# Kernel optimization log

Measured on AMD Instinct MI355X. Metric: run time of the kernel, lower is better.

## Reference

```python
import jax, jax.numpy as jnp
import numpy as np

EMB = 128
N_LIG = 32768
N_REC = 262144
NUM_GRAPHS = 1024
E_LIG = 327680
E_REC = 2097152
LIG_DIMS = [119, 9, 11, 12, 9, 5, 8, 2, 2]
NUM_LAYERS = 3
BN_EPS = 1e-5


def setup_inputs() -> dict:
    key = jax.random.key(0)
    ks = iter(jax.random.split(key, 64))

    lig_x = jnp.stack(
        [jax.random.randint(next(ks), (N_LIG,), 0, d) for d in LIG_DIMS], axis=1
    )  # [N_lig, 9] categorical atom features
    atom_offsets = jnp.asarray(np.cumsum([0] + LIG_DIMS[:-1]), dtype=jnp.int32)
    atom_emb = jax.random.normal(next(ks), (sum(LIG_DIMS), EMB), jnp.float32) * 0.1

    rec_x_int = jax.random.randint(next(ks), (N_REC,), 0, 20)
    rec_x_float = jax.random.normal(next(ks), (N_REC, 199), jnp.float32)
    rec_emb1 = jax.random.normal(next(ks), (20, EMB), jnp.float32) * 0.1
    rec_w = jax.random.normal(next(ks), (199, EMB), jnp.float32) * 0.05
    rec_b = jnp.zeros((EMB,), jnp.float32)

    lig_edge_index = jax.random.randint(next(ks), (2, E_LIG), 0, N_LIG)
    rec_edge_index = jax.random.randint(next(ks), (2, E_REC), 0, N_REC)
    lig_batch = jnp.repeat(jnp.arange(NUM_GRAPHS), N_LIG // NUM_GRAPHS)
    rec_batch = jnp.repeat(jnp.arange(NUM_GRAPHS), N_REC // NUM_GRAPHS)

    def layer_params():
        W = jax.random.normal(next(ks), (NUM_LAYERS, EMB, EMB), jnp.float32) * (1.0 / np.sqrt(EMB))
        b = jnp.zeros((NUM_LAYERS, EMB), jnp.float32)
        gamma = jnp.ones((NUM_LAYERS, EMB), jnp.float32)
        beta = jnp.zeros((NUM_LAYERS, EMB), jnp.float32)
        return W, b, gamma, beta

    lig_W, lig_b, lig_gamma, lig_beta = layer_params()
    rec_W, rec_bc, rec_gamma, rec_beta = layer_params()

    out_w1 = jax.random.normal(next(ks), (2 * EMB, EMB), jnp.float32) * (1.0 / np.sqrt(2 * EMB))
    out_b1 = jnp.zeros((EMB,), jnp.float32)
    out_w2 = jax.random.normal(next(ks), (EMB, 1), jnp.float32) * (1.0 / np.sqrt(EMB))
    out_b2 = jnp.zeros((1,), jnp.float32)

    return dict(
        lig_x=lig_x, rec_x_int=rec_x_int, rec_x_float=rec_x_float,
        lig_edge_index=lig_edge_index, rec_edge_index=rec_edge_index,
        lig_batch=lig_batch, rec_batch=rec_batch, atom_offsets=atom_offsets,
        atom_emb=atom_emb, rec_emb1=rec_emb1, rec_w=rec_w, rec_b=rec_b,
        lig_W=lig_W, lig_b=lig_b, lig_gamma=lig_gamma, lig_beta=lig_beta,
        rec_W=rec_W, rec_bc=rec_bc, rec_gamma=rec_gamma, rec_beta=rec_beta,
        out_w1=out_w1, out_b1=out_b1, out_w2=out_w2, out_b2=out_b2,
    )


def gcn_layer(x, edge_index, W, b, gamma, beta):
    """GCNConv (sym-norm, self loops) -> BatchNorm (batch stats) -> ReLU."""
    n = x.shape[0]
    h = x @ W  # [N, EMB]
    loops = jnp.arange(n)
    src = jnp.concatenate([edge_index[0], loops])
    dst = jnp.concatenate([edge_index[1], loops])
    deg = jax.ops.segment_sum(jnp.ones_like(dst, dtype=h.dtype), dst, num_segments=n)
    dinv = jax.lax.rsqrt(jnp.maximum(deg, 1.0))  # deg >= 1 with self loops
    msg = h[src] * (dinv[src] * dinv[dst])[:, None]  # gather + normalize
    out = jax.ops.segment_sum(msg, dst, num_segments=n) + b
    mu = out.mean(axis=0)
    var = out.var(axis=0)
    out = (out - mu) * jax.lax.rsqrt(var + BN_EPS) * gamma + beta
    return jax.nn.relu(out)


def scatter_mean(x, seg, num_segments):
    s = jax.ops.segment_sum(x, seg, num_segments=num_segments)
    cnt = jax.ops.segment_sum(jnp.ones((x.shape[0],), x.dtype), seg, num_segments=num_segments)
    return s / jnp.maximum(cnt, 1.0)[:, None]


def reference(lig_x, rec_x_int, rec_x_float, lig_edge_index, rec_edge_index,
              lig_batch, rec_batch, atom_offsets, atom_emb, rec_emb1, rec_w, rec_b,
              lig_W, lig_b, lig_gamma, lig_beta, rec_W, rec_bc, rec_gamma, rec_beta,
              out_w1, out_b1, out_w2, out_b2):
    # Node encoders
    lig_h = atom_emb[lig_x + atom_offsets[None, :]].sum(axis=1)        # [N_lig, EMB]
    rec_h = rec_emb1[rec_x_int] + rec_x_float @ rec_w + rec_b          # [N_rec, EMB]

    for l in range(NUM_LAYERS):
        lig_h = gcn_layer(lig_h, lig_edge_index, lig_W[l], lig_b[l], lig_gamma[l], lig_beta[l])
        rec_h = gcn_layer(rec_h, rec_edge_index, rec_W[l], rec_bc[l], rec_gamma[l], rec_beta[l])

    lig_feat = scatter_mean(lig_h, lig_batch, NUM_GRAPHS)
    rec_feat = scatter_mean(rec_h, rec_batch, NUM_GRAPHS)
    z = jnp.concatenate([lig_feat, rec_feat], axis=1)                  # [B, 2*EMB]
    z = jax.nn.relu(z @ out_w1 + out_b1)
    return (z @ out_w2 + out_b2).squeeze(-1)                            # [B]
```

## Files before the change

kernel.cpp:

```cpp
#include <hip/hip_runtime.h>
#include <hip/hip_bf16.h>
#include <cstdint>
#include <cstddef>

#define EMB 128
#define NLIG 32768
#define NREC 262144
#define NGRAPH 1024
#define ELIG 327680
#define EREC 2097152
#define BN_EPS 1e-5f

typedef unsigned short ushort_t;
typedef short bf16x8 __attribute__((ext_vector_type(8)));
typedef float f32x4 __attribute__((ext_vector_type(4)));

__device__ __forceinline__ float bf2f(ushort_t u) {
  union { unsigned int i; float f; } v;
  v.i = ((unsigned int)u) << 16;
  return v.f;
}
__device__ __forceinline__ ushort_t f2bf(float f) {
  __hip_bfloat16 h = __float2bfloat16(f);
  union { __hip_bfloat16 h; ushort_t u; } v;
  v.h = h;
  return v.u;
}


__global__ __launch_bounds__(256)
void gk_count(const int* __restrict__ dst, int* __restrict__ cnt, int E) {
  int e = blockIdx.x * 256 + threadIdx.x;
  if (e < E) atomicAdd(&cnt[dst[e]], 1);
}

__global__ __launch_bounds__(256)
void gk_scan1(const int* __restrict__ cnt, int* __restrict__ off,
              int* __restrict__ bsum, int n) {
  __shared__ int sm[256];
  int t = threadIdx.x;
  int base = blockIdx.x * 1024 + t * 4;
  int v0 = (base + 0 < n) ? cnt[base + 0] : 0;
  int v1 = (base + 1 < n) ? cnt[base + 1] : 0;
  int v2 = (base + 2 < n) ? cnt[base + 2] : 0;
  int v3 = (base + 3 < n) ? cnt[base + 3] : 0;
  int loc = v0 + v1 + v2 + v3;
  sm[t] = loc;
  __syncthreads();
  for (int o = 1; o < 256; o <<= 1) {
    int x = (t >= o) ? sm[t - o] : 0;
    __syncthreads();
    sm[t] += x;
    __syncthreads();
  }
  int run = sm[t] - loc;
  if (base + 0 < n) off[base + 0] = run;
  run += v0;
  if (base + 1 < n) off[base + 1] = run;
  run += v1;
  if (base + 2 < n) off[base + 2] = run;
  run += v2;
  if (base + 3 < n) off[base + 3] = run;
  if (t == 255) bsum[blockIdx.x] = sm[255];
}

__global__ __launch_bounds__(256)
void gk_scan2(int* __restrict__ bsum, int nb) {
  __shared__ int sm[256];
  int t = threadIdx.x;
  int v = (t < nb) ? bsum[t] : 0;
  sm[t] = v;
  __syncthreads();
  for (int o = 1; o < 256; o <<= 1) {
    int x = (t >= o) ? sm[t - o] : 0;
    __syncthreads();
    sm[t] += x;
    __syncthreads();
  }
  if (t < nb) bsum[t] = sm[t] - v;
}

__global__ __launch_bounds__(256)
void gk_scan3f(int* __restrict__ off, const int* __restrict__ bsum,
               int* __restrict__ cur, float* __restrict__ dinv, int n, int E) {
  int i = blockIdx.x * 256 + threadIdx.x;
  if (i < n) {
    int deg = cur[i];
    int o = off[i] + bsum[i >> 10];
    off[i] = o;
    cur[i] = o;
    dinv[i] = rsqrtf((float)(deg + 1));
  }
  if (i == 0) off[n] = E;
}

__global__ __launch_bounds__(256)
void gk_fill(const int* __restrict__ src, const int* __restrict__ dst,
             int* __restrict__ cur, int* __restrict__ csr, int E) {
  int e = blockIdx.x * 256 + threadIdx.x;
  if (e < E) {
    int d = dst[e];
    int pos = atomicAdd(&cur[d], 1);
    csr[pos] = src[e];
  }
}


__global__ __launch_bounds__(256)
void gk_recw2(const float* __restrict__ W, ushort_t* __restrict__ Wt) {
  int idx = blockIdx.x * 256 + threadIdx.x;
  if (idx < 128 * 224) {
    int c = idx / 224, k = idx - c * 224;
    Wt[idx] = (k < 199) ? f2bf(W[(size_t)k * 128 + c]) : (ushort_t)0;
  }
}

__global__ __launch_bounds__(256)
void gk_xcast(const float* __restrict__ X, ushort_t* __restrict__ Xb) {
  const int ITEMS = NREC * 25;
  int stride = gridDim.x * 256;
  for (int v = blockIdx.x * 256 + threadIdx.x; v < ITEMS; v += stride) {
    int row = v / 25, sub = v - row * 25;
    int k0 = sub * 8;
    const float* xr = X + (size_t)row * 199 + k0;
    ushort_t tmp[8];
#pragma unroll
    for (int j = 0; j < 8; ++j) {
      float f = (k0 + j < 199) ? xr[j] : 0.f;
      tmp[j] = f2bf(f);
    }
    *(uint4*)(Xb + (size_t)row * 200 + k0) = *(uint4*)tmp;
  }
}

#define LIGB (NLIG / 2)
__global__ __launch_bounds__(256)
void gk_enc2(const int* __restrict__ lig_x, const int* __restrict__ offs,
             const float* __restrict__ emb,
             const ushort_t* __restrict__ Xb, const int* __restrict__ xi,
             const float* __restrict__ emb1, const ushort_t* __restrict__ Wt,
             const float* __restrict__ b,
             ushort_t* __restrict__ Al, ushort_t* __restrict__ Ar) {
  int t = threadIdx.x;
  if (blockIdx.x < LIGB) {
    __shared__ int idx[2][9];
    int n0 = blockIdx.x * 2;
    if (t < 9) idx[0][t] = lig_x[n0 * 9 + t] + offs[t];
    else if (t >= 128 && t < 137) idx[1][t - 128] = lig_x[(n0 + 1) * 9 + (t - 128)] + offs[t - 128];
    __syncthreads();
    int half = t >> 7, c = t & 127;
    float acc = 0.f;
#pragma unroll
    for (int f = 0; f < 9; ++f) acc += emb[(size_t)idx[half][f] * EMB + c];
    Al[(size_t)(n0 + half) * EMB + c] = f2bf(acc);
    return;
  }
  int row0 = (blockIdx.x - LIGB) * 128;
  int w = t >> 6, lane = t & 63;
  int m = lane & 15, quad = lane >> 4;
  int rbase = w * 32;
  int rA = row0 + rbase + m;
  int rB = rA + 16;

  f32x4 acc[2][8];
#pragma unroll
  for (int rt = 0; rt < 2; ++rt)
#pragma unroll
    for (int ct = 0; ct < 8; ++ct) acc[rt][ct] = (f32x4){0.f, 0.f, 0.f, 0.f};

  const ushort_t* xpA = Xb + (size_t)rA * 200 + quad * 8;
  const ushort_t* xpB = Xb + (size_t)rB * 200 + quad * 8;
  const ushort_t* wp = Wt + (size_t)m * 224 + quad * 8;

  for (int ch = 0; ch < 7; ++ch) {
    bf16x8 a0 = *(const bf16x8*)(xpA + ch * 32);
    bf16x8 a1 = *(const bf16x8*)(xpB + ch * 32);
#pragma unroll
    for (int ct = 0; ct < 8; ++ct) {
      bf16x8 bb = *(const bf16x8*)(wp + (size_t)ct * 16 * 224 + ch * 32);
      acc[0][ct] = __builtin_amdgcn_mfma_f32_16x16x32_bf16(a0, bb, acc[0][ct], 0, 0, 0);
      acc[1][ct] = __builtin_amdgcn_mfma_f32_16x16x32_bf16(a1, bb, acc[1][ct], 0, 0, 0);
    }
  }

  float bcol[8];
#pragma unroll
  for (int ct = 0; ct < 8; ++ct) bcol[ct] = b[ct * 16 + m];
#pragma unroll
  for (int rt = 0; rt < 2; ++rt) {
    int rb = row0 + rbase + rt * 16 + quad * 4;
#pragma unroll
    for (int rr = 0; rr < 4; ++rr) {
      int row = rb + rr;
      const float* e = emb1 + (size_t)xi[row] * 128;
#pragma unroll
      for (int ct = 0; ct < 8; ++ct) {
        int c = ct * 16 + m;
        float v = acc[rt][ct][rr] + bcol[ct] + e[c];
        Ar[(size_t)row * 128 + c] = f2bf(v);
      }
    }
  }
}

__global__ __launch_bounds__(256)
void gk_prep2(const float* __restrict__ Wl, const float* __restrict__ Wr,
              const float* __restrict__ statsAll,
              const float* __restrict__ gml, const float* __restrict__ btl,
              const float* __restrict__ gmr, const float* __restrict__ btr,
              int donorm,
              ushort_t* __restrict__ Wtl, ushort_t* __restrict__ Wtr,
              float* __restrict__ scll, float* __restrict__ shl,
              float* __restrict__ sclr, float* __restrict__ shr) {
  int bidx = blockIdx.x;
  bool isl = bidx < 64;
  const float* W = isl ? Wl : Wr;
  const float* stats = statsAll + (isl ? 0 : 256);
  const float* gamma = isl ? gml : gmr;
  const float* beta = isl ? btl : btr;
  float inv_n = isl ? (1.f / (float)NLIG) : (1.f / (float)NREC);
  ushort_t* Wt = isl ? Wtl : Wtr;
  float* bnscl = isl ? scll : sclr;
  float* bnsh = isl ? shl : shr;
  int idx = (isl ? bidx : bidx - 64) * 256 + threadIdx.x;
  if (idx < 128) {
    if (donorm) {
      float mu = stats[idx] * inv_n;
      float var = stats[128 + idx] * inv_n - mu * mu;
      float s = gamma[idx] * rsqrtf(var + BN_EPS);
      bnscl[idx] = s;
      bnsh[idx] = beta[idx] - mu * s;
    } else {
      bnscl[idx] = 1.f;
      bnsh[idx] = 0.f;
    }
  }
  int c = idx >> 7, k = idx & 127;
  Wt[(size_t)c * 128 + k] = f2bf(W[(size_t)k * 128 + c]);
}

#define MMB_L (NLIG / 128)
__global__ __launch_bounds__(256)
void gk_mm2(const ushort_t* __restrict__ Xl, const ushort_t* __restrict__ Xr,
            const ushort_t* __restrict__ Wtl, const ushort_t* __restrict__ Wtr,
            const float* __restrict__ scll, const float* __restrict__ shl,
            const float* __restrict__ sclr, const float* __restrict__ shr,
            int donorm,
            const float* __restrict__ dinvl, const float* __restrict__ dinvr,
            ushort_t* __restrict__ gbl, ushort_t* __restrict__ gbr) {
  bool isl = blockIdx.x < MMB_L;
  const ushort_t* Xb = isl ? Xl : Xr;
  const ushort_t* Wt = isl ? Wtl : Wtr;
  const float* bnscl = isl ? scll : sclr;
  const float* bnsh = isl ? shl : shr;
  const float* dinv = isl ? dinvl : dinvr;
  ushort_t* gb = isl ? gbl : gbr;
  int row0 = (isl ? blockIdx.x : blockIdx.x - MMB_L) * 128;

  __shared__ ushort_t Xs[128 * 128];
  __shared__ ushort_t Ws[128 * 128];
  int t = threadIdx.x;

  for (int i = t; i < 2048; i += 256) {
    int r = i >> 4, cc = i & 15;
    union { uint4 v; ushort_t s[8]; } u;
    u.v = *(const uint4*)(Xb + (size_t)(row0 + r) * 128 + cc * 8);
    if (donorm) {
#pragma unroll
      for (int j = 0; j < 8; ++j) {
        int k = cc * 8 + j;
        float f = fmaf(bf2f(u.s[j]), bnscl[k], bnsh[k]);
        f = f > 0.f ? f : 0.f;
        u.s[j] = f2bf(f);
      }
    }
    *(uint4*)&Xs[r * 128 + ((cc ^ (r & 15)) * 8)] = u.v;
  }
  for (int i = t; i < 2048; i += 256) {
    int c = i >> 4, cc = i & 15;
    uint4 u = *(const uint4*)(Wt + (size_t)c * 128 + cc * 8);
    *(uint4*)&Ws[c * 128 + ((cc ^ (c & 15)) * 8)] = u;
  }
  __syncthreads();

  int w = t >> 6, lane = t & 63;
  int m = lane & 15, quad = lane >> 4;
  int rbase = w * 32;

  f32x4 acc[2][8];
#pragma unroll
  for (int rt = 0; rt < 2; ++rt)
#pragma unroll
    for (int ct = 0; ct < 8; ++ct) acc[rt][ct] = (f32x4){0.f, 0.f, 0.f, 0.f};

#pragma unroll
  for (int kc8 = 0; kc8 < 16; kc8 += 4) {
    int ck = (kc8 + quad) ^ m;
    bf16x8 a0 = *(const bf16x8*)&Xs[(rbase + m) * 128 + ck * 8];
    bf16x8 a1 = *(const bf16x8*)&Xs[(rbase + 16 + m) * 128 + ck * 8];
#pragma unroll
    for (int ct = 0; ct < 8; ++ct) {
      bf16x8 b = *(const bf16x8*)&Ws[(ct * 16 + m) * 128 + ck * 8];
      acc[0][ct] = __builtin_amdgcn_mfma_f32_16x16x32_bf16(a0, b, acc[0][ct], 0, 0, 0);
      acc[1][ct] = __builtin_amdgcn_mfma_f32_16x16x32_bf16(a1, b, acc[1][ct], 0, 0, 0);
    }
  }

#pragma unroll
  for (int rt = 0; rt < 2; ++rt) {
    int rb = row0 + rbase + rt * 16 + quad * 4;
    float d0 = dinv[rb + 0], d1 = dinv[rb + 1];
    float d2 = dinv[rb + 2], d3 = dinv[rb + 3];
#pragma unroll
    for (int ct = 0; ct < 8; ++ct) {
      int c = ct * 16 + m;
      gb[(size_t)(rb + 0) * 128 + c] = f2bf(acc[rt][ct][0] * d0);
      gb[(size_t)(rb + 1) * 128 + c] = f2bf(acc[rt][ct][1] * d1);
      gb[(size_t)(rb + 2) * 128 + c] = f2bf(acc[rt][ct][2] * d2);
      gb[(size_t)(rb + 3) * 128 + c] = f2bf(acc[rt][ct][3] * d3);
    }
  }
}


__device__ __forceinline__ void gather8(const ushort_t* __restrict__ g, int c0,
                                        int idxv, int q, unsigned int* v) {
#pragma unroll
  for (int k = 0; k < 8; ++k) {
    int idx = __shfl(idxv, q * 8 + k);
    v[k] = *(const unsigned int*)(g + (size_t)idx * 128 + c0);
  }
}

__device__ __forceinline__ void consume8(float2& acc, const unsigned int* v,
                                         int q, int deg) {
#pragma unroll
  for (int k = 0; k < 8; ++k) {
    float m = (q * 8 + k < deg) ? 1.f : 0.f;
    acc.x = fmaf(bf2f((ushort_t)(v[k] & 0xffffu)), m, acc.x);
    acc.y = fmaf(bf2f((ushort_t)(v[k] >> 16)), m, acc.y);
  }
}

#define AGB_L (NLIG / 32)
__global__ __launch_bounds__(256)
void gk_agg2(const ushort_t* __restrict__ gl, const ushort_t* __restrict__ gr,
             const int* __restrict__ offl, const int* __restrict__ offr,
             const int* __restrict__ csrl, const int* __restrict__ csrr,
             const float* __restrict__ dinvl, const float* __restrict__ dinvr,
             ushort_t* __restrict__ outl, ushort_t* __restrict__ outr,
             float* __restrict__ statsAll) {
  bool isl = blockIdx.x < AGB_L;
  const ushort_t* g = isl ? gl : gr;
  const int* off = isl ? offl : offr;
  const int* csr = isl ? csrl : csrr;
  const float* dinv = isl ? dinvl : dinvr;
  ushort_t* outb = isl ? outl : outr;
  float* stats = statsAll + (isl ? 0 : 256);
  int i0 = (isl ? blockIdx.x : blockIdx.x - AGB_L) * 32;

  __shared__ float ls[128];
  __shared__ float lss[128];
  int t = threadIdx.x;
  int slot = t >> 6;
  int lane = t & 63;
  int c0 = lane * 2;

  if (t < 128) { ls[t] = 0.f; lss[t] = 0.f; }
  __syncthreads();

  int offv = off[i0 + min(lane, 32)];

  int idxA[4], idxB[4], dAs[4], dBs[4];
#pragma unroll
  for (int p = 0; p < 4; ++p) {
    int base = slot * 2 + p * 8;
    int eA  = __shfl(offv, base + 0);
    int eB  = __shfl(offv, base + 1);
    int eB1 = __shfl(offv, base + 2);
    dAs[p] = eB - eA;
    dBs[p] = eB1 - eB;
    int adrA = (dAs[p] > 0) ? min(eA + lane, eB - 1) : 0;
    int adrB = (dBs[p] > 0) ? min(eB + lane, eB1 - 1) : 0;
    idxA[p] = csr[adrA];
    idxB[p] = csr[adrB];
  }

  float sx = 0.f, sy = 0.f, ssx = 0.f, ssy = 0.f;

#pragma unroll
  for (int p = 0; p < 4; ++p) {
    int rA = i0 + slot * 2 + p * 8;
    int rB = rA + 1;
    int degA = dAs[p], degB = dBs[p];
    float dA = dinv[rA], dB = dinv[rB];

    unsigned int sU = *(const unsigned int*)(g + (size_t)rA * 128 + c0);
    unsigned int sV = *(const unsigned int*)(g + (size_t)rB * 128 + c0);
    float2 accA = make_float2(bf2f((ushort_t)(sU & 0xffffu)),
                              bf2f((ushort_t)(sU >> 16)));
    float2 accB = make_float2(bf2f((ushort_t)(sV & 0xffffu)),
                              bf2f((ushort_t)(sV >> 16)));

    int dAf = min(degA, 64), dBf = min(degB, 64);
    int nc = (max(dAf, dBf) + 7) >> 3;
    if (nc > 0) {
      unsigned int vA[8], vB[8];
      gather8(g, c0, idxA[p], 0, vA);
      gather8(g, c0, idxB[p], 0, vB);
      for (int q = 1; q < nc; ++q) {
        unsigned int wA[8], wB[8];
        gather8(g, c0, idxA[p], q, wA);
        gather8(g, c0, idxB[p], q, wB);
        consume8(accA, vA, q - 1, dAf);
        consume8(accB, vB, q - 1, dBf);
#pragma unroll
        for (int k = 0; k < 8; ++k) { vA[k] = wA[k]; vB[k] = wB[k]; }
      }
      consume8(accA, vA, nc - 1, dAf);
      consume8(accB, vB, nc - 1, dBf);
    }

    if (degA > 64) {
      int eA = __shfl(offv, slot * 2 + p * 8);
      for (int e = eA + 64; e < eA + degA; ++e) {
        int idx = csr[e];
        unsigned int v = *(const unsigned int*)(g + (size_t)idx * 128 + c0);
        accA.x += bf2f((ushort_t)(v & 0xffffu));
        accA.y += bf2f((ushort_t)(v >> 16));
      }
    }
    if (degB > 64) {
      int eB = __shfl(offv, slot * 2 + p * 8 + 1);
      for (int e = eB + 64; e < eB + degB; ++e) {
        int idx = csr[e];
        unsigned int v = *(const unsigned int*)(g + (size_t)idx * 128 + c0);
        accB.x += bf2f((ushort_t)(v & 0xffffu));
        accB.y += bf2f((ushort_t)(v >> 16));
      }
    }

    accA.x *= dA; accA.y *= dA;
    accB.x *= dB; accB.y *= dB;
    unsigned int oA = (unsigned int)f2bf(accA.x) | ((unsigned int)f2bf(accA.y) << 16);
    unsigned int oB = (unsigned int)f2bf(accB.x) | ((unsigned int)f2bf(accB.y) << 16);
    *(unsigned int*)(outb + (size_t)rA * 128 + c0) = oA;
    *(unsigned int*)(outb + (size_t)rB * 128 + c0) = oB;
    sx += accA.x + accB.x;
    sy += accA.y + accB.y;
    ssx = fmaf(accA.x, accA.x, ssx); ssx = fmaf(accB.x, accB.x, ssx);
    ssy = fmaf(accA.y, accA.y, ssy); ssy = fmaf(accB.y, accB.y, ssy);
  }

  atomicAdd(&ls[c0 + 0], sx);
  atomicAdd(&ls[c0 + 1], sy);
  atomicAdd(&lss[c0 + 0], ssx);
  atomicAdd(&lss[c0 + 1], ssy);
  __syncthreads();
  if (t < 128) {
    atomicAdd(&stats[t], ls[t]);
    atomicAdd(&stats[t + 128], lss[t]);
  }
}

__global__ __launch_bounds__(128)
void gk_pool2(const ushort_t* __restrict__ Al, const ushort_t* __restrict__ Ar,
              const float* __restrict__ statsAll,
              const float* __restrict__ gml, const float* __restrict__ btl,
              const float* __restrict__ gmr, const float* __restrict__ btr,
              float* __restrict__ z) {
  bool isl = blockIdx.x < NGRAPH;
  int gidx = isl ? blockIdx.x : blockIdx.x - NGRAPH;
  const ushort_t* A = isl ? Al : Ar;
  const float* stats = statsAll + (isl ? 0 : 256);
  const float* gamma = isl ? gml : gmr;
  const float* beta = isl ? btl : btr;
  float inv_n = isl ? (1.f / (float)NLIG) : (1.f / (float)NREC);
  int npg = isl ? (NLIG / NGRAPH) : (NREC / NGRAPH);
  int zoff = isl ? 0 : EMB;

  int c = threadIdx.x;
  float mu = stats[c] * inv_n;
  float var = stats[128 + c] * inv_n - mu * mu;
  float scl = gamma[c] * rsqrtf(var + BN_EPS);
  float be = beta[c];
  float sum = 0.f;
  int r0 = gidx * npg;
  for (int r = 0; r < npg; ++r) {
    float v = (bf2f(A[(size_t)(r0 + r) * 128 + c]) - mu) * scl + be;
    sum += v > 0.f ? v : 0.f;
  }
  z[(size_t)gidx * 256 + zoff + c] = sum * (1.0f / (float)npg);
}

__global__ __launch_bounds__(128)
void gk_mlp(const float* __restrict__ z, const float* __restrict__ w1,
            const float* __restrict__ b1, const float* __restrict__ w2,
            const float* __restrict__ b2, float* __restrict__ out) {
  __shared__ float zs[256];
  __shared__ float red[128];
  int gidx = blockIdx.x, t = threadIdx.x;
  zs[t] = z[(size_t)gidx * 256 + t];
  zs[t + 128] = z[(size_t)gidx * 256 + 128 + t];
  __syncthreads();
  float acc = b1[t];
  for (int k = 0; k < 256; ++k) acc += zs[k] * w1[(size_t)k * 128 + t];
  acc = (acc > 0.f ? acc : 0.f) * w2[t];
  red[t] = acc;
  __syncthreads();
  for (int o = 64; o > 0; o >>= 1) {
    if (t < o) red[t] += red[t + o];
    __syncthreads();
  }
  if (t == 0) out[gidx] = red[0] + b2[0];
}


extern "C" void kernel_launch(void* const* d_in, const int* in_sizes, int n_in,
                              void* d_out, int out_size, void* d_ws, size_t ws_size,
                              hipStream_t stream) {
  (void)in_sizes; (void)n_in; (void)out_size; (void)ws_size;
  const int*   lig_x       = (const int*)  d_in[0];
  const int*   rec_x_int   = (const int*)  d_in[1];
  const float* rec_x_float = (const float*)d_in[2];
  const int*   lig_ei      = (const int*)  d_in[3];
  const int*   rec_ei      = (const int*)  d_in[4];
  const int*   atom_off    = (const int*)  d_in[7];
  const float* atom_emb    = (const float*)d_in[8];
  const float* rec_emb1    = (const float*)d_in[9];
  const float* rec_w       = (const float*)d_in[10];
  const float* rec_b       = (const float*)d_in[11];
  const float* lig_W       = (const float*)d_in[12];
  const float* lig_gamma   = (const float*)d_in[14];
  const float* lig_beta    = (const float*)d_in[15];
  const float* rec_W       = (const float*)d_in[16];
  const float* rec_gamma   = (const float*)d_in[18];
  const float* rec_beta    = (const float*)d_in[19];
  const float* out_w1      = (const float*)d_in[20];
  const float* out_b1      = (const float*)d_in[21];
  const float* out_w2      = (const float*)d_in[22];
  const float* out_b2      = (const float*)d_in[23];
  float* out = (float*)d_out;

  char* p = (char*)d_ws;
  auto alloc = [&](size_t bytes) -> void* {
    void* r = p;
    p += (bytes + 255) & ~(size_t)255;
    return r;
  };
  ushort_t* Ab_r   = (ushort_t*)alloc((size_t)NREC * EMB * 2);
  ushort_t* Gb_r   = (ushort_t*)alloc((size_t)NREC * EMB * 2);
  ushort_t* Ab_l   = (ushort_t*)alloc((size_t)NLIG * EMB * 2);
  ushort_t* Gb_l   = (ushort_t*)alloc((size_t)NLIG * EMB * 2);
  ushort_t* Wtb_l  = (ushort_t*)alloc((size_t)EMB * EMB * 2);
  ushort_t* Wtb_r  = (ushort_t*)alloc((size_t)EMB * EMB * 2);
  ushort_t* WtK    = (ushort_t*)alloc((size_t)EMB * 224 * 2);
  ushort_t* Xb2    = (ushort_t*)alloc(((size_t)NREC * 200 + 64) * 2);
  float* scl_l     = (float*)alloc(128 * 4);
  float* sh_l      = (float*)alloc(128 * 4);
  float* scl_r     = (float*)alloc(128 * 4);
  float* sh_r      = (float*)alloc(128 * 4);
  float* dinv_lig  = (float*)alloc((size_t)NLIG * 4);
  float* dinv_rec  = (float*)alloc((size_t)NREC * 4);
  int*   cnt_lig   = (int*)  alloc((size_t)NLIG * 4);
  int*   cnt_rec   = (int*)  alloc((size_t)NREC * 4);
  int*   off_lig   = (int*)  alloc((size_t)(NLIG + 8) * 4);
  int*   off_rec   = (int*)  alloc((size_t)(NREC + 8) * 4);
  int*   csr_lig   = (int*)  alloc((size_t)ELIG * 4);
  int*   csr_rec   = (int*)  alloc((size_t)EREC * 4);
  int*   bsum_lig  = (int*)  alloc(256 * 4);
  int*   bsum_rec  = (int*)  alloc(256 * 4);
  float* stats2    = (float*)alloc(512 * 4);
  float* z         = (float*)alloc((size_t)NGRAPH * 256 * 4);

  hipMemsetAsync(cnt_lig, 0, (size_t)NLIG * 4, stream);
  hipMemsetAsync(cnt_rec, 0, (size_t)NREC * 4, stream);
  gk_count<<<ELIG / 256, 256, 0, stream>>>(lig_ei + ELIG, cnt_lig, ELIG);
  gk_count<<<EREC / 256, 256, 0, stream>>>(rec_ei + EREC, cnt_rec, EREC);
  gk_scan1<<<NLIG / 1024, 256, 0, stream>>>(cnt_lig, off_lig, bsum_lig, NLIG);
  gk_scan2<<<1, 256, 0, stream>>>(bsum_lig, NLIG / 1024);
  gk_scan3f<<<NLIG / 256, 256, 0, stream>>>(off_lig, bsum_lig, cnt_lig,
                                            dinv_lig, NLIG, ELIG);
  gk_scan1<<<NREC / 1024, 256, 0, stream>>>(cnt_rec, off_rec, bsum_rec, NREC);
  gk_scan2<<<1, 256, 0, stream>>>(bsum_rec, NREC / 1024);
  gk_scan3f<<<NREC / 256, 256, 0, stream>>>(off_rec, bsum_rec, cnt_rec,
                                            dinv_rec, NREC, EREC);
  gk_fill<<<ELIG / 256, 256, 0, stream>>>(lig_ei, lig_ei + ELIG, cnt_lig, csr_lig, ELIG);
  gk_fill<<<EREC / 256, 256, 0, stream>>>(rec_ei, rec_ei + EREC, cnt_rec, csr_rec, EREC);

  gk_recw2<<<112, 256, 0, stream>>>(rec_w, WtK);
  gk_xcast<<<2048, 256, 0, stream>>>(rec_x_float, Xb2);
  gk_enc2<<<LIGB + NREC / 128, 256, 0, stream>>>(lig_x, atom_off, atom_emb,
                                                 Xb2, rec_x_int, rec_emb1,
                                                 WtK, rec_b, Ab_l, Ab_r);

  for (int l = 0; l < 3; ++l) {
    const float* Wl = lig_W + (size_t)l * EMB * EMB;
    const float* Wr = rec_W + (size_t)l * EMB * EMB;
    const float* gml = (l > 0) ? lig_gamma + (size_t)(l - 1) * EMB : lig_gamma;
    const float* btl = (l > 0) ? lig_beta + (size_t)(l - 1) * EMB : lig_beta;
    const float* gmr = (l > 0) ? rec_gamma + (size_t)(l - 1) * EMB : rec_gamma;
    const float* btr = (l > 0) ? rec_beta + (size_t)(l - 1) * EMB : rec_beta;
    gk_prep2<<<128, 256, 0, stream>>>(Wl, Wr, stats2, gml, btl, gmr, btr,
                                      l > 0 ? 1 : 0, Wtb_l, Wtb_r,
                                      scl_l, sh_l, scl_r, sh_r);
    hipMemsetAsync(stats2, 0, 512 * 4, stream);
    gk_mm2<<<MMB_L + NREC / 128, 256, 0, stream>>>(
        Ab_l, Ab_r, Wtb_l, Wtb_r, scl_l, sh_l, scl_r, sh_r, l > 0 ? 1 : 0,
        dinv_lig, dinv_rec, Gb_l, Gb_r);
    gk_agg2<<<AGB_L + NREC / 32, 256, 0, stream>>>(
        Gb_l, Gb_r, off_lig, off_rec, csr_lig, csr_rec,
        dinv_lig, dinv_rec, Ab_l, Ab_r, stats2);
  }

  gk_pool2<<<2 * NGRAPH, 128, 0, stream>>>(Ab_l, Ab_r, stats2,
                                           lig_gamma + 2 * EMB, lig_beta + 2 * EMB,
                                           rec_gamma + 2 * EMB, rec_beta + 2 * EMB, z);
  gk_mlp<<<NGRAPH, 128, 0, stream>>>(z, out_w1, out_b1, out_w2, out_b2, out);
}
```

Measured before the change: 1.795 ms.

## Merge preprocessing kernels into horizontally fused multi-role launches

Combines the degree-count, weight cast and input cast into one launch, the two scans per graph into joint launches, and the CSR fill together with the node encoders into one launch, with the role chosen by block index. This takes the preprocessing from thirteen dependent launches down to five, so there are fewer launch gaps and independent work can run side by side. The fused encoder kernel now holds the GEMM blocks together with the atomic fill blocks, which may hurt occupancy or register allocation for the GEMM path.

```diff
diff --git a/kernel.cpp b/kernel.cpp
--- a/kernel.cpp
+++ b/kernel.cpp
@@ -28,18 +28,60 @@
 }
 
 
-__global__ __launch_bounds__(256)
-void gk_count(const int* __restrict__ dst, int* __restrict__ cnt, int E) {
-  int e = blockIdx.x * 256 + threadIdx.x;
-  if (e < E) atomicAdd(&cnt[dst[e]], 1);
-}
-
-__global__ __launch_bounds__(256)
-void gk_scan1(const int* __restrict__ cnt, int* __restrict__ off,
-              int* __restrict__ bsum, int n) {
-  __shared__ int sm[256];
+#define PA_CL (ELIG / 256)
+#define PA_CR (EREC / 256)
+#define PA_CW 112
+#define PA_CX 2048
+__global__ __launch_bounds__(256)
+void gk_phaseA(const int* __restrict__ lig_dst, const int* __restrict__ rec_dst,
+               int* __restrict__ cnt_l, int* __restrict__ cnt_r,
+               const float* __restrict__ W, ushort_t* __restrict__ Wt,
+               const float* __restrict__ X, ushort_t* __restrict__ Xb) {
+  int b = blockIdx.x;
   int t = threadIdx.x;
-  int base = blockIdx.x * 1024 + t * 4;
+  if (b < PA_CL) {
+    int e = b * 256 + t;
+    atomicAdd(&cnt_l[lig_dst[e]], 1);
+    return;
+  }
+  b -= PA_CL;
+  if (b < PA_CR) {
+    int e = b * 256 + t;
+    atomicAdd(&cnt_r[rec_dst[e]], 1);
+    return;
+  }
+  b -= PA_CR;
+  if (b < PA_CW) {
+    int idx = b * 256 + t;
+    if (idx < 128 * 224) {
+      int c = idx / 224, k = idx - c * 224;
+      Wt[idx] = (k < 199) ? f2bf(W[(size_t)k * 128 + c]) : (ushort_t)0;
+    }
+    return;
+  }
+  b -= PA_CW;
+  const int ITEMS = NREC * 25;
+  int stride = PA_CX * 256;
+  for (int v = b * 256 + t; v < ITEMS; v += stride) {
+    int row = v / 25, sub = v - row * 25;
+    int k0 = sub * 8;
+    const float* xr = X + (size_t)row * 199 + k0;
+    ushort_t tmp[8];
+#pragma unroll
+    for (int j = 0; j < 8; ++j) {
+      float f = (k0 + j < 199) ? xr[j] : 0.f;
+      tmp[j] = f2bf(f);
+    }
+    *(uint4*)(Xb + (size_t)row * 200 + k0) = *(uint4*)tmp;
+  }
+}
+
+__device__ __forceinline__ void scan1_body(const int* __restrict__ cnt,
+                                           int* __restrict__ off,
+                                           int* __restrict__ bsum,
+                                           int n, int blk, int* sm) {
+  int t = threadIdx.x;
+  int base = blk * 1024 + t * 4;
   int v0 = (base + 0 < n) ? cnt[base + 0] : 0;
   int v1 = (base + 1 < n) ? cnt[base + 1] : 0;
   int v2 = (base + 2 < n) ? cnt[base + 2] : 0;
@@ -61,12 +103,24 @@
   if (base + 2 < n) off[base + 2] = run;
   run += v2;
   if (base + 3 < n) off[base + 3] = run;
-  if (t == 255) bsum[blockIdx.x] = sm[255];
-}
-
-__global__ __launch_bounds__(256)
-void gk_scan2(int* __restrict__ bsum, int nb) {
+  if (t == 255) bsum[blk] = sm[255];
+}
+
+#define S1_L (NLIG / 1024)
+#define S1_R (NREC / 1024)
+__global__ __launch_bounds__(256)
+void gk_scan1b(const int* __restrict__ cnt_l, int* __restrict__ off_l,
+               int* __restrict__ bsum_l,
+               const int* __restrict__ cnt_r, int* __restrict__ off_r,
+               int* __restrict__ bsum_r) {
   __shared__ int sm[256];
+  int b = blockIdx.x;
+  if (b < S1_L) scan1_body(cnt_l, off_l, bsum_l, NLIG, b, sm);
+  else          scan1_body(cnt_r, off_r, bsum_r, NREC, b - S1_L, sm);
+}
+
+__device__ __forceinline__ void scan2_body(int* __restrict__ bsum, int nb,
+                                           int* sm) {
   int t = threadIdx.x;
   int v = (t < nb) ? bsum[t] : 0;
   sm[t] = v;
@@ -81,9 +135,18 @@
 }
 
 __global__ __launch_bounds__(256)
-void gk_scan3f(int* __restrict__ off, const int* __restrict__ bsum,
-               int* __restrict__ cur, float* __restrict__ dinv, int n, int E) {
-  int i = blockIdx.x * 256 + threadIdx.x;
+void gk_scan2b(int* __restrict__ bsum_l, int* __restrict__ bsum_r) {
+  __shared__ int sm[256];
+  if (blockIdx.x == 0) scan2_body(bsum_l, S1_L, sm);
+  else                 scan2_body(bsum_r, S1_R, sm);
+}
+
+__device__ __forceinline__ void scan3_body(int* __restrict__ off,
+                                           const int* __restrict__ bsum,
+                                           int* __restrict__ cur,
+                                           float* __restrict__ dinv,
+                                           int n, int E, int blk) {
+  int i = blk * 256 + threadIdx.x;
   if (i < n) {
     int deg = cur[i];
     int o = off[i] + bsum[i >> 10];
@@ -94,57 +157,52 @@
   if (i == 0) off[n] = E;
 }
 
-__global__ __launch_bounds__(256)
-void gk_fill(const int* __restrict__ src, const int* __restrict__ dst,
-             int* __restrict__ cur, int* __restrict__ csr, int E) {
-  int e = blockIdx.x * 256 + threadIdx.x;
-  if (e < E) {
-    int d = dst[e];
-    int pos = atomicAdd(&cur[d], 1);
-    csr[pos] = src[e];
-  }
-}
-
-
-__global__ __launch_bounds__(256)
-void gk_recw2(const float* __restrict__ W, ushort_t* __restrict__ Wt) {
-  int idx = blockIdx.x * 256 + threadIdx.x;
-  if (idx < 128 * 224) {
-    int c = idx / 224, k = idx - c * 224;
-    Wt[idx] = (k < 199) ? f2bf(W[(size_t)k * 128 + c]) : (ushort_t)0;
-  }
-}
-
-__global__ __launch_bounds__(256)
-void gk_xcast(const float* __restrict__ X, ushort_t* __restrict__ Xb) {
-  const int ITEMS = NREC * 25;
-  int stride = gridDim.x * 256;
-  for (int v = blockIdx.x * 256 + threadIdx.x; v < ITEMS; v += stride) {
-    int row = v / 25, sub = v - row * 25;
-    int k0 = sub * 8;
-    const float* xr = X + (size_t)row * 199 + k0;
-    ushort_t tmp[8];
-#pragma unroll
-    for (int j = 0; j < 8; ++j) {
-      float f = (k0 + j < 199) ? xr[j] : 0.f;
-      tmp[j] = f2bf(f);
-    }
-    *(uint4*)(Xb + (size_t)row * 200 + k0) = *(uint4*)tmp;
-  }
-}
-
+#define S3_L (NLIG / 256)
+#define S3_R (NREC / 256)
+__global__ __launch_bounds__(256)
+void gk_scan3b(int* __restrict__ off_l, const int* __restrict__ bsum_l,
+               int* __restrict__ cur_l, float* __restrict__ dinv_l,
+               int* __restrict__ off_r, const int* __restrict__ bsum_r,
+               int* __restrict__ cur_r, float* __restrict__ dinv_r) {
+  int b = blockIdx.x;
+  if (b < S3_L) scan3_body(off_l, bsum_l, cur_l, dinv_l, NLIG, ELIG, b);
+  else          scan3_body(off_r, bsum_r, cur_r, dinv_r, NREC, EREC, b - S3_L);
+}
+
+#define PE_FL (ELIG / 256)
+#define PE_FR (EREC / 256)
 #define LIGB (NLIG / 2)
 __global__ __launch_bounds__(256)
-void gk_enc2(const int* __restrict__ lig_x, const int* __restrict__ offs,
-             const float* __restrict__ emb,
-             const ushort_t* __restrict__ Xb, const int* __restrict__ xi,
-             const float* __restrict__ emb1, const ushort_t* __restrict__ Wt,
-             const float* __restrict__ b,
-             ushort_t* __restrict__ Al, ushort_t* __restrict__ Ar) {
+void gk_phaseE(const int* __restrict__ lig_ei, const int* __restrict__ rec_ei,
+               int* __restrict__ cur_l, int* __restrict__ cur_r,
+               int* __restrict__ csr_l, int* __restrict__ csr_r,
+               const int* __restrict__ lig_x, const int* __restrict__ offs,
+               const float* __restrict__ emb,
+               const ushort_t* __restrict__ Xb, const int* __restrict__ xi,
+               const float* __restrict__ emb1, const ushort_t* __restrict__ Wt,
+               const float* __restrict__ b,
+               ushort_t* __restrict__ Al, ushort_t* __restrict__ Ar) {
+  int blk = blockIdx.x;
   int t = threadIdx.x;
-  if (blockIdx.x < LIGB) {
+  if (blk < PE_FL) {
+    int e = blk * 256 + t;
+    int d = lig_ei[ELIG + e];
+    int pos = atomicAdd(&cur_l[d], 1);
+    csr_l[pos] = lig_ei[e];
+    return;
+  }
+  blk -= PE_FL;
+  if (blk < PE_FR) {
+    int e = blk * 256 + t;
+    int d = rec_ei[EREC + e];
+    int pos = atomicAdd(&cur_r[d], 1);
+    csr_r[pos] = rec_ei[e];
+    return;
+  }
+  blk -= PE_FR;
+  if (blk < LIGB) {
     __shared__ int idx[2][9];
-    int n0 = blockIdx.x * 2;
+    int n0 = blk * 2;
     if (t < 9) idx[0][t] = lig_x[n0 * 9 + t] + offs[t];
     else if (t >= 128 && t < 137) idx[1][t - 128] = lig_x[(n0 + 1) * 9 + (t - 128)] + offs[t - 128];
     __syncthreads();
@@ -155,7 +213,7 @@
     Al[(size_t)(n0 + half) * EMB + c] = f2bf(acc);
     return;
   }
-  int row0 = (blockIdx.x - LIGB) * 128;
+  int row0 = (blk - LIGB) * 128;
   int w = t >> 6, lane = t & 63;
   int m = lane & 15, quad = lane >> 4;
   int rbase = w * 32;
@@ -575,24 +633,18 @@
 
   hipMemsetAsync(cnt_lig, 0, (size_t)NLIG * 4, stream);
   hipMemsetAsync(cnt_rec, 0, (size_t)NREC * 4, stream);
-  gk_count<<<ELIG / 256, 256, 0, stream>>>(lig_ei + ELIG, cnt_lig, ELIG);
-  gk_count<<<EREC / 256, 256, 0, stream>>>(rec_ei + EREC, cnt_rec, EREC);
-  gk_scan1<<<NLIG / 1024, 256, 0, stream>>>(cnt_lig, off_lig, bsum_lig, NLIG);
-  gk_scan2<<<1, 256, 0, stream>>>(bsum_lig, NLIG / 1024);
-  gk_scan3f<<<NLIG / 256, 256, 0, stream>>>(off_lig, bsum_lig, cnt_lig,
-                                            dinv_lig, NLIG, ELIG);
-  gk_scan1<<<NREC / 1024, 256, 0, stream>>>(cnt_rec, off_rec, bsum_rec, NREC);
-  gk_scan2<<<1, 256, 0, stream>>>(bsum_rec, NREC / 1024);
-  gk_scan3f<<<NREC / 256, 256, 0, stream>>>(off_rec, bsum_rec, cnt_rec,
-                                            dinv_rec, NREC, EREC);
-  gk_fill<<<ELIG / 256, 256, 0, stream>>>(lig_ei, lig_ei + ELIG, cnt_lig, csr_lig, ELIG);
-  gk_fill<<<EREC / 256, 256, 0, stream>>>(rec_ei, rec_ei + EREC, cnt_rec, csr_rec, EREC);
-
-  gk_recw2<<<112, 256, 0, stream>>>(rec_w, WtK);
-  gk_xcast<<<2048, 256, 0, stream>>>(rec_x_float, Xb2);
-  gk_enc2<<<LIGB + NREC / 128, 256, 0, stream>>>(lig_x, atom_off, atom_emb,
-                                                 Xb2, rec_x_int, rec_emb1,
-                                                 WtK, rec_b, Ab_l, Ab_r);
+  gk_phaseA<<<PA_CL + PA_CR + PA_CW + PA_CX, 256, 0, stream>>>(
+      lig_ei + ELIG, rec_ei + EREC, cnt_lig, cnt_rec, rec_w, WtK,
+      rec_x_float, Xb2);
+  gk_scan1b<<<S1_L + S1_R, 256, 0, stream>>>(cnt_lig, off_lig, bsum_lig,
+                                             cnt_rec, off_rec, bsum_rec);
+  gk_scan2b<<<2, 256, 0, stream>>>(bsum_lig, bsum_rec);
+  gk_scan3b<<<S3_L + S3_R, 256, 0, stream>>>(off_lig, bsum_lig, cnt_lig, dinv_lig,
+                                             off_rec, bsum_rec, cnt_rec, dinv_rec);
+  gk_phaseE<<<PE_FL + PE_FR + LIGB + NREC / 128, 256, 0, stream>>>(
+      lig_ei, rec_ei, cnt_lig, cnt_rec, csr_lig, csr_rec,
+      lig_x, atom_off, atom_emb, Xb2, rec_x_int, rec_emb1, WtK, rec_b,
+      Ab_l, Ab_r);
 
   for (int l = 0; l < 3; ++l) {
     const float* Wl = lig_W + (size_t)l * EMB * EMB;
```

Result: faster. 1.733 ms (-3.4%).
